# Kernel tuning notes

Measured on AMD Instinct MI355X. Metric: run time of the kernel, lower is better.

The kernel has to match this reference:

```python
import jax, jax.numpy as jnp
import numpy as np

B, D, NT, NZ = 16384, 64, 128, 2048


def setup_inputs() -> dict:
    key = jax.random.key(0)
    ks = jax.random.split(key, 5)
    return {
        "t": jax.random.uniform(ks[0], (1,), dtype=jnp.float32),
        "z": jax.random.normal(ks[1], (B, D), dtype=jnp.float32),
        "logp_z": jnp.zeros((B, 1), jnp.float32),
        "centres_z": jax.random.normal(ks[2], (NZ, D), dtype=jnp.float32),
        "log_sigmas_z": jnp.zeros((NZ,), jnp.float32),
        "centres_t": jax.random.normal(ks[3], (NT, 1), dtype=jnp.float32),
        "log_sigmas_t": jnp.zeros((NT,), jnp.float32),
        "W": 0.01 * jax.random.normal(ks[4], (D, NT, NZ + 1), dtype=jnp.float32),
    }


def _gauss(r):
    return jnp.exp(-r * r)


def _forward(t, z, centres_z, log_sigmas_z, centres_t, log_sigmas_t, W):
    # time RBF features Phi_t: (NT,)
    r_t = jnp.abs(t.reshape(1, 1) - centres_t.reshape(1, -1)) / jnp.exp(log_sigmas_t)
    phi_t = _gauss(r_t).reshape(-1)
    W_t = jnp.einsum('dij,i->dj', W, phi_t)  # (D, NZ+1)
    Wz, bias = W_t[:, :-1], W_t[:, -1]       # bias comes from the appended ones column
    # z RBF features via squared-distance identity (avoids [B,NZ,D] blowup)
    sq = (jnp.sum(z * z, axis=1, keepdims=True)
          + jnp.sum(centres_z * centres_z, axis=1)[None, :]
          - 2.0 * z @ centres_z.T)
    sq = jnp.maximum(sq, 0.0)                 # (B, NZ) squared distances
    inv_s2 = jnp.exp(-2.0 * log_sigmas_z)     # 1/sigma_j^2, (NZ,)
    phi_z = jnp.exp(-sq * inv_s2)             # gaussian(||z-c_j||/s_j), (B, NZ)
    dz_dt = phi_z @ Wz.T + bias               # (B, D)
    # exact Jacobian trace for gaussian basis:
    #   d phi_j / d z_i = -2 * phi_j * (z_i - c_{j,i}) / s_j^2
    #   tr(J)_b = sum_j phi_{b,j} * inv_s2_j * (-2) * (sum_i Wz[i,j] z_{b,i} - sum_i Wz[i,j] c_{j,i})
    q = jnp.einsum('dj,jd->j', Wz, centres_z)  # (NZ,)
    trace = -2.0 * jnp.sum(phi_z * inv_s2 * (z @ Wz - q), axis=1)  # (B,)
    dlogp_z_dt = -trace[:, None]               # (B, 1)
    return dz_dt, dlogp_z_dt


def reference(t, z, logp_z, centres_z, log_sigmas_z, centres_t, log_sigmas_t, W):
    return _forward(t, z, centres_z, log_sigmas_z, centres_t, log_sigmas_t, W)
```

## Files before the change

kernel.cpp:

```cpp
#include <hip/hip_runtime.h>
#include <math.h>

typedef unsigned int uint;
typedef unsigned short ushort;
typedef unsigned char uchar;
typedef __attribute__((ext_vector_type(4))) float f32x4;

#define BB  16384
#define DD  64
#define NT_ 128
#define NZ_ 2048
#define NJ_ 2049

#define BIAS_OFF 0
#define SCS_OFF  64
#define ZF8A_OFF 8256
#define ZF8B_OFF 139328
#define ZZG_OFF  270400
#define CZ8A_OFF 286784
#define CZ8B_OFF 303168
#define WZ8A_OFF 319552
#define WZ8B_OFF 335936
#define WZBP_OFF 352320
#define PART_OFF 417856

#if __has_builtin(__builtin_amdgcn_cvt_pk_fp8_f32)
__device__ __forceinline__ uint pk4_fp8(float a, float b, float c, float d) {
  int v = __builtin_amdgcn_cvt_pk_fp8_f32(a, b, 0, false);
  v = __builtin_amdgcn_cvt_pk_fp8_f32(c, d, v, true);
  return (uint)v;
}
__device__ __forceinline__ uchar f8_1(float x) {
  return (uchar)(__builtin_amdgcn_cvt_pk_fp8_f32(x, x, 0, false) & 0xFF);
}
#else
__device__ __forceinline__ uint sw_f8(float x) {
  uint u = __float_as_uint(x);
  uint s = (u >> 24) & 0x80u;
  float ax = __uint_as_float(u & 0x7FFFFFFFu);
  if (!(ax >= 0.015625f)) return s;
  if (ax >= 448.f) return s | 0x7Eu;
  uint q = __float_as_uint(ax);
  q += 0x7FFFFu + ((q >> 20) & 1u);
  uint e = (q >> 23) - 120u;
  return s | ((e & 0xFu) << 3) | ((q >> 20) & 7u);
}
__device__ __forceinline__ uchar f8_1(float x) { return (uchar)sw_f8(x); }
__device__ __forceinline__ uint pk4_fp8(float a, float b, float c, float d) {
  return sw_f8(a) | (sw_f8(b) << 8) | (sw_f8(c) << 16) | (sw_f8(d) << 24);
}
#endif

__global__ __launch_bounds__(256) void k_wt1(
    const float* __restrict__ t, const float* __restrict__ ct,
    const float* __restrict__ lst, const float* __restrict__ W,
    float* __restrict__ part)
{
  __shared__ float ph[32];
  int tx = threadIdx.x;
  int d  = blockIdx.y;
  int ic = blockIdx.z;
  if (tx < 32) {
    int i = ic * 32 + tx;
    float r = fabsf(t[0] - ct[i]) * __expf(-lst[i]);
    ph[tx] = __expf(-r * r);
  }
  __syncthreads();
  int j = blockIdx.x * 256 + tx;
  if (j >= NJ_) return;
  const float* Wp = W + (size_t)d * NT_ * NJ_ + (size_t)(ic * 32) * NJ_ + j;
  float acc = 0.f;
#pragma unroll
  for (int k = 0; k < 32; ++k) acc += Wp[(size_t)k * NJ_] * ph[k];
  part[((size_t)ic * 64 + d) * NJ_ + j] = acc;
}

__global__ __launch_bounds__(256) void k_prep2(
    const float* __restrict__ part, const float* __restrict__ cz,
    const float* __restrict__ lsz,
    float* __restrict__ bias, float4* __restrict__ scs,
    uchar* __restrict__ cz8a, uchar* __restrict__ cz8b,
    uchar* __restrict__ wz8a, uchar* __restrict__ wz8b,
    uchar* __restrict__ wzbp8)
{
  __shared__ float wt[64][9];
  int tid = threadIdx.x;
  int cb0 = blockIdx.x * 8;
#pragma unroll
  for (int h = 0; h < 2; ++h) {
    int f = h * 256 + tid;
    int d = f >> 3, c = f & 7;
    size_t idx = (size_t)d * NJ_ + cb0 + c;
    float s = part[idx] + part[(size_t)64 * NJ_ + idx]
            + part[(size_t)128 * NJ_ + idx] + part[(size_t)192 * NJ_ + idx];
    wt[d][c] = s;
    int cg = cb0 + c;
    wzbp8[((size_t)(cg >> 5) * 64 + d) * 32 + (cg & 31)] = f8_1(s);
  }
  if (blockIdx.x == 0 && tid < 64) {
    size_t idx = (size_t)tid * NJ_ + 2048;
    bias[tid] = part[idx] + part[(size_t)64 * NJ_ + idx]
              + part[(size_t)128 * NJ_ + idx] + part[(size_t)192 * NJ_ + idx];
  }
  __syncthreads();
  int cl = tid >> 5;
  int k  = tid & 31;
  int c  = cb0 + cl;
  float cv0 = cz[(size_t)c * DD + k];
  float cv1 = cz[(size_t)c * DD + 32 + k];
  cz8a[(size_t)c * 32 + k] = f8_1(cv0);
  cz8b[(size_t)c * 32 + k] = f8_1(cv1);
  float w0 = wt[k][cl], w1 = wt[32 + k][cl];
  wz8a[(size_t)c * 32 + k] = f8_1(w0);
  wz8b[(size_t)c * 32 + k] = f8_1(w1);
  float ca = cv0 * cv0 + cv1 * cv1;
  float qa = w0 * cv0 + w1 * cv1;
  qa += __shfl_xor(qa, 1);  ca += __shfl_xor(ca, 1);
  qa += __shfl_xor(qa, 2);  ca += __shfl_xor(ca, 2);
  qa += __shfl_xor(qa, 4);  ca += __shfl_xor(ca, 4);
  qa += __shfl_xor(qa, 8);  ca += __shfl_xor(ca, 8);
  qa += __shfl_xor(qa, 16); ca += __shfl_xor(ca, 16);
  if (k == 0) scs[c] = make_float4(ca, __expf(-2.f * lsz[c]), qa, 0.f);
}

__global__ __launch_bounds__(256) void k_zbp(
    const float* __restrict__ z, uchar* __restrict__ zf8a,
    uchar* __restrict__ zf8b, float* __restrict__ zzg)
{
  int g = blockIdx.x * 256 + threadIdx.x;
  int r = g >> 3, s8 = g & 7;
  const float4* zp = (const float4*)(z + (size_t)r * DD + s8 * 8);
  float4 v0 = zp[0], v1 = zp[1];
  uint lo = pk4_fp8(v0.x, v0.y, v0.z, v0.w);
  uint hi = pk4_fp8(v1.x, v1.y, v1.z, v1.w);
  uchar* dst = (s8 < 4 ? zf8a : zf8b) + (size_t)r * 32 + (s8 & 3) * 8;
  *(uint2*)dst = make_uint2(lo, hi);
  float ss = v0.x * v0.x + v0.y * v0.y + v0.z * v0.z + v0.w * v0.w
           + v1.x * v1.x + v1.y * v1.y + v1.z * v1.z + v1.w * v1.w;
  ss += __shfl_xor(ss, 1);
  ss += __shfl_xor(ss, 2);
  ss += __shfl_xor(ss, 4);
  if (s8 == 0) zzg[r] = ss;
}

#define PH_LD 40

__global__ __launch_bounds__(256) void k_fused(
    const uchar* __restrict__ zf8a, const uchar* __restrict__ zf8b,
    const float* __restrict__ zzg,
    const uchar* __restrict__ cz8a, const uchar* __restrict__ cz8b,
    const uchar* __restrict__ wz8a, const uchar* __restrict__ wz8b,
    const uchar* __restrict__ wzbp8,
    const float4* __restrict__ scs, const float* __restrict__ bias,
    float* __restrict__ out)
{
  __shared__ char smem[10240];
  __shared__ float dlr[4][32];
  uchar* phs = (uchar*)smem;
  float* eps = (float*)smem;

  int tid  = threadIdx.x;
  int ws   = tid >> 6;
  int lane = tid & 63;
  int lrow = lane & 15, quad = lane >> 4;
  int b0 = blockIdx.x * 32;

  long az[2][2];
#pragma unroll
  for (int mt = 0; mt < 2; ++mt) {
    size_t ro = (size_t)(b0 + mt * 16 + lrow) * 32 + quad * 8;
    az[mt][0] = *(const long*)(zf8a + ro);
    az[mt][1] = *(const long*)(zf8b + ro);
  }
  float zzr[2][4];
#pragma unroll
  for (int mt = 0; mt < 2; ++mt) {
    float v = zzg[b0 + mt * 16 + lrow];
#pragma unroll
    for (int i = 0; i < 4; ++i) zzr[mt][i] = __shfl(v, quad * 4 + i);
  }

  f32x4 acc[2][4];
#pragma unroll
  for (int mt = 0; mt < 2; ++mt)
#pragma unroll
    for (int nt = 0; nt < 4; ++nt) acc[mt][nt] = (f32x4){0.f, 0.f, 0.f, 0.f};
  float dl[2][4] = {{0.f}};

  const f32x4 zero = (f32x4){0.f, 0.f, 0.f, 0.f};
  int cbase = ws * 512;
  int pbase = ws * 32 * PH_LD;

  long Abc0[2][2], Abc1[2][2], Abw0[2][2], Abw1[2][2], Abb[2][4];
  float4 Asc[2][2];
#define LOADB(PAR, C0)                                                         \
  do {                                                                         \
    int c0_ = (C0);                                                            \
    _Pragma("unroll")                                                          \
    for (int nt = 0; nt < 2; ++nt) {                                           \
      int cg_ = c0_ + nt * 16 + lrow;                                          \
      size_t ro_ = (size_t)cg_ * 32 + quad * 8;                                \
      Abc0[PAR][nt] = *(const long*)(cz8a + ro_);                              \
      Abc1[PAR][nt] = *(const long*)(cz8b + ro_);                              \
      Abw0[PAR][nt] = *(const long*)(wz8a + ro_);                              \
      Abw1[PAR][nt] = *(const long*)(wz8b + ro_);                              \
      Asc[PAR][nt]  = scs[cg_];                                                \
    }                                                                          \
    size_t cb_ = (size_t)(c0_ >> 5) * 64 * 32;                                 \
    _Pragma("unroll")                                                          \
    for (int nt = 0; nt < 4; ++nt)                                             \
      Abb[PAR][nt] =                                                           \
          *(const long*)(wzbp8 + cb_ + (size_t)(nt * 16 + lrow) * 32 + quad * 8); \
  } while (0)

  LOADB(0, cbase);
#pragma unroll 2
  for (int it = 0; it < 16; ++it) {
    int par = it & 1;
    LOADB(par ^ 1, cbase + ((it + 1) & 15) * 32);

    int pb = par * (4 * 32 * PH_LD) + pbase;
#pragma unroll
    for (int nt = 0; nt < 2; ++nt) {
      float4 sc = Asc[par][nt];
#pragma unroll
      for (int mt = 0; mt < 2; ++mt) {
        f32x4 d1 = __builtin_amdgcn_mfma_f32_16x16x32_fp8_fp8(az[mt][0], Abc0[par][nt], zero, 0, 0, 0);
        d1       = __builtin_amdgcn_mfma_f32_16x16x32_fp8_fp8(az[mt][1], Abc1[par][nt], d1,   0, 0, 0);
        f32x4 d2 = __builtin_amdgcn_mfma_f32_16x16x32_fp8_fp8(az[mt][0], Abw0[par][nt], zero, 0, 0, 0);
        d2       = __builtin_amdgcn_mfma_f32_16x16x32_fp8_fp8(az[mt][1], Abw1[par][nt], d2,   0, 0, 0);
#pragma unroll
        for (int i = 0; i < 4; ++i) {
          float s = zzr[mt][i] + sc.x - 2.f * d1[i];
          s = fmaxf(s, 0.f);
          float p = __expf(-s * sc.y);
          dl[mt][i] += p * sc.y * (d2[i] - sc.z);
          phs[pb + (mt * 16 + quad * 4 + i) * PH_LD + nt * 16 + lrow] = f8_1(p);
        }
      }
    }
    long ap0 = *(const long*)&phs[pb + lrow * PH_LD + quad * 8];
    long ap1 = *(const long*)&phs[pb + (16 + lrow) * PH_LD + quad * 8];
#pragma unroll
    for (int nt = 0; nt < 4; ++nt) {
      acc[0][nt] = __builtin_amdgcn_mfma_f32_16x16x32_fp8_fp8(ap0, Abb[par][nt], acc[0][nt], 0, 0, 0);
      acc[1][nt] = __builtin_amdgcn_mfma_f32_16x16x32_fp8_fp8(ap1, Abb[par][nt], acc[1][nt], 0, 0, 0);
    }
  }
#undef LOADB

#pragma unroll
  for (int mt = 0; mt < 2; ++mt)
#pragma unroll
    for (int i = 0; i < 4; ++i) {
      float v = dl[mt][i];
      v += __shfl_xor(v, 1);
      v += __shfl_xor(v, 2);
      v += __shfl_xor(v, 4);
      v += __shfl_xor(v, 8);
      if (lrow == 0) dlr[ws][mt * 16 + quad * 4 + i] = v;
    }

  for (int s = 0; s < 4; ++s) {
    __syncthreads();
    if (ws == s) {
#pragma unroll
      for (int mt = 0; mt < 2; ++mt)
#pragma unroll
        for (int nt = 0; nt < 4; ++nt)
#pragma unroll
          for (int i = 0; i < 4; ++i) {
            int r = mt * 16 + quad * 4 + i;
            int d = nt * 16 + lrow;
            if (s == 0) eps[r * 68 + d] = acc[mt][nt][i];
            else        eps[r * 68 + d] += acc[mt][nt][i];
          }
    }
  }
  __syncthreads();

  {
    int r = tid >> 3, d0 = (tid & 7) * 8;
    float4 e0 = *(const float4*)&eps[r * 68 + d0];
    float4 e1 = *(const float4*)&eps[r * 68 + d0 + 4];
    float4 bv0 = *(const float4*)&bias[d0];
    float4 bv1 = *(const float4*)&bias[d0 + 4];
    float4 o0, o1;
    o0.x = e0.x + bv0.x; o0.y = e0.y + bv0.y; o0.z = e0.z + bv0.z; o0.w = e0.w + bv0.w;
    o1.x = e1.x + bv1.x; o1.y = e1.y + bv1.y; o1.z = e1.z + bv1.z; o1.w = e1.w + bv1.w;
    *(float4*)&out[(size_t)(b0 + r) * DD + d0]     = o0;
    *(float4*)&out[(size_t)(b0 + r) * DD + d0 + 4] = o1;
  }
  if (tid < 32) {
    float s = dlr[0][tid] + dlr[1][tid] + dlr[2][tid] + dlr[3][tid];
    out[(size_t)BB * DD + b0 + tid] = 2.f * s;
  }
}

extern "C" void kernel_launch(void* const* d_in, const int* in_sizes, int n_in,
                              void* d_out, int out_size, void* d_ws, size_t ws_size,
                              hipStream_t stream)
{
  const float* t   = (const float*)d_in[0];
  const float* z   = (const float*)d_in[1];
  const float* cz  = (const float*)d_in[3];
  const float* lsz = (const float*)d_in[4];
  const float* ct  = (const float*)d_in[5];
  const float* lst = (const float*)d_in[6];
  const float* W   = (const float*)d_in[7];
  float* out = (float*)d_out;
  float* ws  = (float*)d_ws;

  float*  bias = ws + BIAS_OFF;
  float4* scs  = (float4*)(ws + SCS_OFF);
  uchar*  zf8a = (uchar*)(ws + ZF8A_OFF);
  uchar*  zf8b = (uchar*)(ws + ZF8B_OFF);
  float*  zzg  = ws + ZZG_OFF;
  uchar*  cz8a = (uchar*)(ws + CZ8A_OFF);
  uchar*  cz8b = (uchar*)(ws + CZ8B_OFF);
  uchar*  wz8a = (uchar*)(ws + WZ8A_OFF);
  uchar*  wz8b = (uchar*)(ws + WZ8B_OFF);
  uchar*  wzbp8 = (uchar*)(ws + WZBP_OFF);
  float*  part = ws + PART_OFF;

  k_wt1<<<dim3(9, 64, 4), 256, 0, stream>>>(t, ct, lst, W, part);
  k_prep2<<<dim3(256), 256, 0, stream>>>(part, cz, lsz, bias, scs,
                                         cz8a, cz8b, wz8a, wz8b, wzbp8);
  k_zbp<<<dim3(512), 256, 0, stream>>>(z, zf8a, zf8b, zzg);
  k_fused<<<dim3(BB / 32), 256, 0, stream>>>(zf8a, zf8b, zzg, cz8a, cz8b,
                                             wz8a, wz8b, wzbp8, scs, bias, out);
}
```

Baseline: 141.2 us.

## Fuse z fp8 packing into main kernel and halve rows per block

Removes the separate k_zbp pass. The main kernel now loads fp32 z directly, converts it to fp8 in registers and computes row norms with cross-quad shuffles, which drops a launch and a workspace round-trip. It also halves the batch tile from 32 to 16 rows per block, doubling the grid and shrinking shared memory and register state. The trade-off is that each centre and weight fragment is reused across only 16 rows, so L2 and global traffic for the fp8 centre and weight data roughly doubles.

After: 151.3 us. 1.07x slower.

```diff
diff --git a/kernel.cpp b/kernel.cpp
--- a/kernel.cpp
+++ b/kernel.cpp
@@ -2,7 +2,7 @@
 #include <math.h>
 
 typedef unsigned int uint;
-typedef unsigned short ushort;
+typedef unsigned long ulong;
 typedef unsigned char uchar;
 typedef __attribute__((ext_vector_type(4))) float f32x4;
 
@@ -14,15 +14,12 @@
 
 #define BIAS_OFF 0
 #define SCS_OFF  64
-#define ZF8A_OFF 8256
-#define ZF8B_OFF 139328
-#define ZZG_OFF  270400
-#define CZ8A_OFF 286784
-#define CZ8B_OFF 303168
-#define WZ8A_OFF 319552
-#define WZ8B_OFF 335936
-#define WZBP_OFF 352320
-#define PART_OFF 417856
+#define CZ8A_OFF 8256
+#define CZ8B_OFF 24640
+#define WZ8A_OFF 41024
+#define WZ8B_OFF 57408
+#define WZBP_OFF 73792
+#define PART_OFF 106560
 
 #if __has_builtin(__builtin_amdgcn_cvt_pk_fp8_f32)
 __device__ __forceinline__ uint pk4_fp8(float a, float b, float c, float d) {
@@ -123,39 +120,18 @@
   if (k == 0) scs[c] = make_float4(ca, __expf(-2.f * lsz[c]), qa, 0.f);
 }
 
-__global__ __launch_bounds__(256) void k_zbp(
-    const float* __restrict__ z, uchar* __restrict__ zf8a,
-    uchar* __restrict__ zf8b, float* __restrict__ zzg)
-{
-  int g = blockIdx.x * 256 + threadIdx.x;
-  int r = g >> 3, s8 = g & 7;
-  const float4* zp = (const float4*)(z + (size_t)r * DD + s8 * 8);
-  float4 v0 = zp[0], v1 = zp[1];
-  uint lo = pk4_fp8(v0.x, v0.y, v0.z, v0.w);
-  uint hi = pk4_fp8(v1.x, v1.y, v1.z, v1.w);
-  uchar* dst = (s8 < 4 ? zf8a : zf8b) + (size_t)r * 32 + (s8 & 3) * 8;
-  *(uint2*)dst = make_uint2(lo, hi);
-  float ss = v0.x * v0.x + v0.y * v0.y + v0.z * v0.z + v0.w * v0.w
-           + v1.x * v1.x + v1.y * v1.y + v1.z * v1.z + v1.w * v1.w;
-  ss += __shfl_xor(ss, 1);
-  ss += __shfl_xor(ss, 2);
-  ss += __shfl_xor(ss, 4);
-  if (s8 == 0) zzg[r] = ss;
-}
-
 #define PH_LD 40
 
 __global__ __launch_bounds__(256) void k_fused(
-    const uchar* __restrict__ zf8a, const uchar* __restrict__ zf8b,
-    const float* __restrict__ zzg,
+    const float* __restrict__ z,
     const uchar* __restrict__ cz8a, const uchar* __restrict__ cz8b,
     const uchar* __restrict__ wz8a, const uchar* __restrict__ wz8b,
     const uchar* __restrict__ wzbp8,
     const float4* __restrict__ scs, const float* __restrict__ bias,
     float* __restrict__ out)
 {
-  __shared__ char smem[10240];
-  __shared__ float dlr[4][32];
+  __shared__ char smem[5376];
+  __shared__ float dlr[4][16];
   uchar* phs = (uchar*)smem;
   float* eps = (float*)smem;
 
@@ -163,33 +139,40 @@
   int ws   = tid >> 6;
   int lane = tid & 63;
   int lrow = lane & 15, quad = lane >> 4;
-  int b0 = blockIdx.x * 32;
-
-  long az[2][2];
-#pragma unroll
-  for (int mt = 0; mt < 2; ++mt) {
-    size_t ro = (size_t)(b0 + mt * 16 + lrow) * 32 + quad * 8;
-    az[mt][0] = *(const long*)(zf8a + ro);
-    az[mt][1] = *(const long*)(zf8b + ro);
-  }
-  float zzr[2][4];
-#pragma unroll
-  for (int mt = 0; mt < 2; ++mt) {
-    float v = zzg[b0 + mt * 16 + lrow];
-#pragma unroll
-    for (int i = 0; i < 4; ++i) zzr[mt][i] = __shfl(v, quad * 4 + i);
-  }
-
-  f32x4 acc[2][4];
-#pragma unroll
-  for (int mt = 0; mt < 2; ++mt)
-#pragma unroll
-    for (int nt = 0; nt < 4; ++nt) acc[mt][nt] = (f32x4){0.f, 0.f, 0.f, 0.f};
-  float dl[2][4] = {{0.f}};
+  int b0 = blockIdx.x * 16;
+
+  long az[2];
+  float zzr[4];
+  {
+    const float* zr = z + (size_t)(b0 + lrow) * DD + quad * 8;
+    float4 u0 = *(const float4*)(zr);
+    float4 u1 = *(const float4*)(zr + 4);
+    float4 u2 = *(const float4*)(zr + 32);
+    float4 u3 = *(const float4*)(zr + 36);
+    uint l0 = pk4_fp8(u0.x, u0.y, u0.z, u0.w);
+    uint h0 = pk4_fp8(u1.x, u1.y, u1.z, u1.w);
+    uint l1 = pk4_fp8(u2.x, u2.y, u2.z, u2.w);
+    uint h1 = pk4_fp8(u3.x, u3.y, u3.z, u3.w);
+    az[0] = (long)((ulong)l0 | ((ulong)h0 << 32));
+    az[1] = (long)((ulong)l1 | ((ulong)h1 << 32));
+    float p = u0.x*u0.x + u0.y*u0.y + u0.z*u0.z + u0.w*u0.w
+            + u1.x*u1.x + u1.y*u1.y + u1.z*u1.z + u1.w*u1.w
+            + u2.x*u2.x + u2.y*u2.y + u2.z*u2.z + u2.w*u2.w
+            + u3.x*u3.x + u3.y*u3.y + u3.z*u3.z + u3.w*u3.w;
+    p += __shfl_xor(p, 16);
+    p += __shfl_xor(p, 32);
+#pragma unroll
+    for (int i = 0; i < 4; ++i) zzr[i] = __shfl(p, quad * 4 + i);
+  }
+
+  f32x4 acc[4];
+#pragma unroll
+  for (int nt = 0; nt < 4; ++nt) acc[nt] = (f32x4){0.f, 0.f, 0.f, 0.f};
+  float dl[4] = {0.f, 0.f, 0.f, 0.f};
 
   const f32x4 zero = (f32x4){0.f, 0.f, 0.f, 0.f};
   int cbase = ws * 512;
-  int pbase = ws * 32 * PH_LD;
+  int pbase = ws * 16 * PH_LD;
 
   long Abc0[2][2], Abc1[2][2], Abw0[2][2], Abw1[2][2], Abb[2][4];
   float4 Asc[2][2];
@@ -219,79 +202,65 @@
     int par = it & 1;
     LOADB(par ^ 1, cbase + ((it + 1) & 15) * 32);
 
-    int pb = par * (4 * 32 * PH_LD) + pbase;
+    int pb = par * (4 * 16 * PH_LD) + pbase;
 #pragma unroll
     for (int nt = 0; nt < 2; ++nt) {
       float4 sc = Asc[par][nt];
-#pragma unroll
-      for (int mt = 0; mt < 2; ++mt) {
-        f32x4 d1 = __builtin_amdgcn_mfma_f32_16x16x32_fp8_fp8(az[mt][0], Abc0[par][nt], zero, 0, 0, 0);
-        d1       = __builtin_amdgcn_mfma_f32_16x16x32_fp8_fp8(az[mt][1], Abc1[par][nt], d1,   0, 0, 0);
-        f32x4 d2 = __builtin_amdgcn_mfma_f32_16x16x32_fp8_fp8(az[mt][0], Abw0[par][nt], zero, 0, 0, 0);
-        d2       = __builtin_amdgcn_mfma_f32_16x16x32_fp8_fp8(az[mt][1], Abw1[par][nt], d2,   0, 0, 0);
-#pragma unroll
-        for (int i = 0; i < 4; ++i) {
-          float s = zzr[mt][i] + sc.x - 2.f * d1[i];
-          s = fmaxf(s, 0.f);
-          float p = __expf(-s * sc.y);
-          dl[mt][i] += p * sc.y * (d2[i] - sc.z);
-          phs[pb + (mt * 16 + quad * 4 + i) * PH_LD + nt * 16 + lrow] = f8_1(p);
-        }
+      f32x4 d1 = __builtin_amdgcn_mfma_f32_16x16x32_fp8_fp8(az[0], Abc0[par][nt], zero, 0, 0, 0);
+      d1       = __builtin_amdgcn_mfma_f32_16x16x32_fp8_fp8(az[1], Abc1[par][nt], d1,   0, 0, 0);
+      f32x4 d2 = __builtin_amdgcn_mfma_f32_16x16x32_fp8_fp8(az[0], Abw0[par][nt], zero, 0, 0, 0);
+      d2       = __builtin_amdgcn_mfma_f32_16x16x32_fp8_fp8(az[1], Abw1[par][nt], d2,   0, 0, 0);
+#pragma unroll
+      for (int i = 0; i < 4; ++i) {
+        float s = zzr[i] + sc.x - 2.f * d1[i];
+        s = fmaxf(s, 0.f);
+        float p = __expf(-s * sc.y);
+        dl[i] += p * sc.y * (d2[i] - sc.z);
+        phs[pb + (quad * 4 + i) * PH_LD + nt * 16 + lrow] = f8_1(p);
       }
     }
-    long ap0 = *(const long*)&phs[pb + lrow * PH_LD + quad * 8];
-    long ap1 = *(const long*)&phs[pb + (16 + lrow) * PH_LD + quad * 8];
-#pragma unroll
-    for (int nt = 0; nt < 4; ++nt) {
-      acc[0][nt] = __builtin_amdgcn_mfma_f32_16x16x32_fp8_fp8(ap0, Abb[par][nt], acc[0][nt], 0, 0, 0);
-      acc[1][nt] = __builtin_amdgcn_mfma_f32_16x16x32_fp8_fp8(ap1, Abb[par][nt], acc[1][nt], 0, 0, 0);
-    }
+    long ap = *(const long*)&phs[pb + lrow * PH_LD + quad * 8];
+#pragma unroll
+    for (int nt = 0; nt < 4; ++nt)
+      acc[nt] = __builtin_amdgcn_mfma_f32_16x16x32_fp8_fp8(ap, Abb[par][nt], acc[nt], 0, 0, 0);
   }
 #undef LOADB
 
 #pragma unroll
-  for (int mt = 0; mt < 2; ++mt)
-#pragma unroll
-    for (int i = 0; i < 4; ++i) {
-      float v = dl[mt][i];
-      v += __shfl_xor(v, 1);
-      v += __shfl_xor(v, 2);
-      v += __shfl_xor(v, 4);
-      v += __shfl_xor(v, 8);
-      if (lrow == 0) dlr[ws][mt * 16 + quad * 4 + i] = v;
-    }
+  for (int i = 0; i < 4; ++i) {
+    float v = dl[i];
+    v += __shfl_xor(v, 1);
+    v += __shfl_xor(v, 2);
+    v += __shfl_xor(v, 4);
+    v += __shfl_xor(v, 8);
+    if (lrow == 0) dlr[ws][quad * 4 + i] = v;
+  }
 
   for (int s = 0; s < 4; ++s) {
     __syncthreads();
     if (ws == s) {
 #pragma unroll
-      for (int mt = 0; mt < 2; ++mt)
-#pragma unroll
-        for (int nt = 0; nt < 4; ++nt)
-#pragma unroll
-          for (int i = 0; i < 4; ++i) {
-            int r = mt * 16 + quad * 4 + i;
-            int d = nt * 16 + lrow;
-            if (s == 0) eps[r * 68 + d] = acc[mt][nt][i];
-            else        eps[r * 68 + d] += acc[mt][nt][i];
-          }
+      for (int nt = 0; nt < 4; ++nt)
+#pragma unroll
+        for (int i = 0; i < 4; ++i) {
+          int r = quad * 4 + i;
+          int d = nt * 16 + lrow;
+          if (s == 0) eps[r * 68 + d] = acc[nt][i];
+          else        eps[r * 68 + d] += acc[nt][i];
+        }
     }
   }
   __syncthreads();
 
   {
-    int r = tid >> 3, d0 = (tid & 7) * 8;
-    float4 e0 = *(const float4*)&eps[r * 68 + d0];
-    float4 e1 = *(const float4*)&eps[r * 68 + d0 + 4];
-    float4 bv0 = *(const float4*)&bias[d0];
-    float4 bv1 = *(const float4*)&bias[d0 + 4];
-    float4 o0, o1;
-    o0.x = e0.x + bv0.x; o0.y = e0.y + bv0.y; o0.z = e0.z + bv0.z; o0.w = e0.w + bv0.w;
-    o1.x = e1.x + bv1.x; o1.y = e1.y + bv1.y; o1.z = e1.z + bv1.z; o1.w = e1.w + bv1.w;
-    *(float4*)&out[(size_t)(b0 + r) * DD + d0]     = o0;
-    *(float4*)&out[(size_t)(b0 + r) * DD + d0 + 4] = o1;
-  }
-  if (tid < 32) {
+    int r = tid >> 4, d0 = (tid & 15) * 4;
+    float4 e  = *(const float4*)&eps[r * 68 + d0];
+    float4 bv = *(const float4*)&bias[d0];
+    float4 o;
+    o.x = e.x + bv.x; o.y = e.y + bv.y; o.z = e.z + bv.z; o.w = e.w + bv.w;
+    *(float4*)&out[(size_t)(b0 + r) * DD + d0] = o;
+  }
+  if (tid < 16) {
     float s = dlr[0][tid] + dlr[1][tid] + dlr[2][tid] + dlr[3][tid];
     out[(size_t)BB * DD + b0 + tid] = 2.f * s;
   }
@@ -313,9 +282,6 @@
 
   float*  bias = ws + BIAS_OFF;
   float4* scs  = (float4*)(ws + SCS_OFF);
-  uchar*  zf8a = (uchar*)(ws + ZF8A_OFF);
-  uchar*  zf8b = (uchar*)(ws + ZF8B_OFF);
-  float*  zzg  = ws + ZZG_OFF;
   uchar*  cz8a = (uchar*)(ws + CZ8A_OFF);
   uchar*  cz8b = (uchar*)(ws + CZ8B_OFF);
   uchar*  wz8a = (uchar*)(ws + WZ8A_OFF);
@@ -326,7 +292,6 @@
   k_wt1<<<dim3(9, 64, 4), 256, 0, stream>>>(t, ct, lst, W, part);
   k_prep2<<<dim3(256), 256, 0, stream>>>(part, cz, lsz, bias, scs,
                                          cz8a, cz8b, wz8a, wz8b, wzbp8);
-  k_zbp<<<dim3(512), 256, 0, stream>>>(z, zf8a, zf8b, zzg);
-  k_fused<<<dim3(BB / 32), 256, 0, stream>>>(zf8a, zf8b, zzg, cz8a, cz8b,
-                                             wz8a, wz8b, wzbp8, scs, bias, out);
-}
+  k_fused<<<dim3(BB / 16), 256, 0, stream>>>(z, cz8a, cz8b, wz8a, wz8b,
+                                             wzbp8, scs, bias, out);
+}
```

## Fuse z fp8 packing into main kernel and transpose MFMA operands for packed stores

Applied to the files above, without the earlier changes.

Removes the separate z-conversion kernel: the fused kernel now reads fp32 z directly, packs it to fp8 and computes row norms in registers. It swaps the MFMA A/B operands so each lane holds four consecutive centres for one row, which allows per-centre constants to be loaded as float4 vectors and the phi values to be stored to LDS as packed 32-bit words instead of single bytes. The float4 struct-of-params layout is split into separate arrays, and the main loop is fully unrolled. This saves one launch and a workspace round-trip at the cost of more redundant z loads per block and higher register pressure.

Measured after the change: 176.1 us. 1.25x slower.

```diff
diff --git a/kernel.cpp b/kernel.cpp
--- a/kernel.cpp
+++ b/kernel.cpp
@@ -2,9 +2,10 @@
 #include <math.h>
 
 typedef unsigned int uint;
-typedef unsigned short ushort;
+typedef unsigned long ulong;
 typedef unsigned char uchar;
 typedef __attribute__((ext_vector_type(4))) float f32x4;
+typedef uint __attribute__((may_alias)) uint_a;
 
 #define BB  16384
 #define DD  64
@@ -13,16 +14,15 @@
 #define NJ_ 2049
 
 #define BIAS_OFF 0
-#define SCS_OFF  64
-#define ZF8A_OFF 8256
-#define ZF8B_OFF 139328
-#define ZZG_OFF  270400
-#define CZ8A_OFF 286784
-#define CZ8B_OFF 303168
-#define WZ8A_OFF 319552
-#define WZ8B_OFF 335936
-#define WZBP_OFF 352320
-#define PART_OFF 417856
+#define CCS_OFF  64
+#define INVS_OFF 2112
+#define QS_OFF   4160
+#define CZ8A_OFF 6208
+#define CZ8B_OFF 22592
+#define WZ8A_OFF 38976
+#define WZ8B_OFF 55360
+#define WZBP_OFF 71744
+#define PART_OFF 104512
 
 #if __has_builtin(__builtin_amdgcn_cvt_pk_fp8_f32)
 __device__ __forceinline__ uint pk4_fp8(float a, float b, float c, float d) {
@@ -78,7 +78,8 @@
 __global__ __launch_bounds__(256) void k_prep2(
     const float* __restrict__ part, const float* __restrict__ cz,
     const float* __restrict__ lsz,
-    float* __restrict__ bias, float4* __restrict__ scs,
+    float* __restrict__ bias, float* __restrict__ ccs,
+    float* __restrict__ invs, float* __restrict__ qs,
     uchar* __restrict__ cz8a, uchar* __restrict__ cz8b,
     uchar* __restrict__ wz8a, uchar* __restrict__ wz8b,
     uchar* __restrict__ wzbp8)
@@ -120,38 +121,22 @@
   qa += __shfl_xor(qa, 4);  ca += __shfl_xor(ca, 4);
   qa += __shfl_xor(qa, 8);  ca += __shfl_xor(ca, 8);
   qa += __shfl_xor(qa, 16); ca += __shfl_xor(ca, 16);
-  if (k == 0) scs[c] = make_float4(ca, __expf(-2.f * lsz[c]), qa, 0.f);
-}
-
-__global__ __launch_bounds__(256) void k_zbp(
-    const float* __restrict__ z, uchar* __restrict__ zf8a,
-    uchar* __restrict__ zf8b, float* __restrict__ zzg)
-{
-  int g = blockIdx.x * 256 + threadIdx.x;
-  int r = g >> 3, s8 = g & 7;
-  const float4* zp = (const float4*)(z + (size_t)r * DD + s8 * 8);
-  float4 v0 = zp[0], v1 = zp[1];
-  uint lo = pk4_fp8(v0.x, v0.y, v0.z, v0.w);
-  uint hi = pk4_fp8(v1.x, v1.y, v1.z, v1.w);
-  uchar* dst = (s8 < 4 ? zf8a : zf8b) + (size_t)r * 32 + (s8 & 3) * 8;
-  *(uint2*)dst = make_uint2(lo, hi);
-  float ss = v0.x * v0.x + v0.y * v0.y + v0.z * v0.z + v0.w * v0.w
-           + v1.x * v1.x + v1.y * v1.y + v1.z * v1.z + v1.w * v1.w;
-  ss += __shfl_xor(ss, 1);
-  ss += __shfl_xor(ss, 2);
-  ss += __shfl_xor(ss, 4);
-  if (s8 == 0) zzg[r] = ss;
+  if (k == 0) {
+    ccs[c]  = ca;
+    invs[c] = __expf(-2.f * lsz[c]);
+    qs[c]   = qa;
+  }
 }
 
 #define PH_LD 40
 
 __global__ __launch_bounds__(256) void k_fused(
-    const uchar* __restrict__ zf8a, const uchar* __restrict__ zf8b,
-    const float* __restrict__ zzg,
+    const float* __restrict__ z,
     const uchar* __restrict__ cz8a, const uchar* __restrict__ cz8b,
     const uchar* __restrict__ wz8a, const uchar* __restrict__ wz8b,
     const uchar* __restrict__ wzbp8,
-    const float4* __restrict__ scs, const float* __restrict__ bias,
+    const float* __restrict__ ccs, const float* __restrict__ invs,
+    const float* __restrict__ qs, const float* __restrict__ bias,
     float* __restrict__ out)
 {
   __shared__ char smem[10240];
@@ -166,18 +151,27 @@
   int b0 = blockIdx.x * 32;
 
   long az[2][2];
+  float zzs[2];
 #pragma unroll
   for (int mt = 0; mt < 2; ++mt) {
-    size_t ro = (size_t)(b0 + mt * 16 + lrow) * 32 + quad * 8;
-    az[mt][0] = *(const long*)(zf8a + ro);
-    az[mt][1] = *(const long*)(zf8b + ro);
-  }
-  float zzr[2][4];
-#pragma unroll
-  for (int mt = 0; mt < 2; ++mt) {
-    float v = zzg[b0 + mt * 16 + lrow];
-#pragma unroll
-    for (int i = 0; i < 4; ++i) zzr[mt][i] = __shfl(v, quad * 4 + i);
+    const float* zr = z + (size_t)(b0 + mt * 16 + lrow) * DD;
+    float4 u0 = *(const float4*)(zr + quad * 8);
+    float4 u1 = *(const float4*)(zr + quad * 8 + 4);
+    float4 u2 = *(const float4*)(zr + 32 + quad * 8);
+    float4 u3 = *(const float4*)(zr + 32 + quad * 8 + 4);
+    uint l0 = pk4_fp8(u0.x, u0.y, u0.z, u0.w);
+    uint h0 = pk4_fp8(u1.x, u1.y, u1.z, u1.w);
+    uint l1 = pk4_fp8(u2.x, u2.y, u2.z, u2.w);
+    uint h1 = pk4_fp8(u3.x, u3.y, u3.z, u3.w);
+    az[mt][0] = (long)((ulong)l0 | ((ulong)h0 << 32));
+    az[mt][1] = (long)((ulong)l1 | ((ulong)h1 << 32));
+    float p = u0.x*u0.x + u0.y*u0.y + u0.z*u0.z + u0.w*u0.w
+            + u1.x*u1.x + u1.y*u1.y + u1.z*u1.z + u1.w*u1.w
+            + u2.x*u2.x + u2.y*u2.y + u2.z*u2.z + u2.w*u2.w
+            + u3.x*u3.x + u3.y*u3.y + u3.z*u3.z + u3.w*u3.w;
+    p += __shfl_xor(p, 16);
+    p += __shfl_xor(p, 32);
+    zzs[mt] = p;
   }
 
   f32x4 acc[2][4];
@@ -185,14 +179,13 @@
   for (int mt = 0; mt < 2; ++mt)
 #pragma unroll
     for (int nt = 0; nt < 4; ++nt) acc[mt][nt] = (f32x4){0.f, 0.f, 0.f, 0.f};
-  float dl[2][4] = {{0.f}};
+  float dl[2] = {0.f, 0.f};
 
   const f32x4 zero = (f32x4){0.f, 0.f, 0.f, 0.f};
   int cbase = ws * 512;
-  int pbase = ws * 32 * PH_LD;
+  int pwave = ws * 2 * 16 * PH_LD;
 
   long Abc0[2][2], Abc1[2][2], Abw0[2][2], Abw1[2][2], Abb[2][4];
-  float4 Asc[2][2];
 #define LOADB(PAR, C0)                                                         \
   do {                                                                         \
     int c0_ = (C0);                                                            \
@@ -204,7 +197,6 @@
       Abc1[PAR][nt] = *(const long*)(cz8b + ro_);                              \
       Abw0[PAR][nt] = *(const long*)(wz8a + ro_);                              \
       Abw1[PAR][nt] = *(const long*)(wz8b + ro_);                              \
-      Asc[PAR][nt]  = scs[cg_];                                                \
     }                                                                          \
     size_t cb_ = (size_t)(c0_ >> 5) * 64 * 32;                                 \
     _Pragma("unroll")                                                          \
@@ -214,52 +206,62 @@
   } while (0)
 
   LOADB(0, cbase);
-#pragma unroll 2
+#pragma unroll
   for (int it = 0; it < 16; ++it) {
-    int par = it & 1;
-    LOADB(par ^ 1, cbase + ((it + 1) & 15) * 32);
-
-    int pb = par * (4 * 32 * PH_LD) + pbase;
+    const int par = it & 1;
+    const int c0 = cbase + it * 32;
+    LOADB(par ^ 1, (it == 15) ? cbase : (c0 + 32));
+
+    const int pb = par * 5120 + pwave;
 #pragma unroll
     for (int nt = 0; nt < 2; ++nt) {
-      float4 sc = Asc[par][nt];
+      int cs = c0 + nt * 16 + quad * 4;
+      f32x4 cc4 = *(const f32x4*)(ccs + cs);
+      f32x4 iv4 = *(const f32x4*)(invs + cs);
+      f32x4 q4  = *(const f32x4*)(qs + cs);
 #pragma unroll
       for (int mt = 0; mt < 2; ++mt) {
-        f32x4 d1 = __builtin_amdgcn_mfma_f32_16x16x32_fp8_fp8(az[mt][0], Abc0[par][nt], zero, 0, 0, 0);
-        d1       = __builtin_amdgcn_mfma_f32_16x16x32_fp8_fp8(az[mt][1], Abc1[par][nt], d1,   0, 0, 0);
-        f32x4 d2 = __builtin_amdgcn_mfma_f32_16x16x32_fp8_fp8(az[mt][0], Abw0[par][nt], zero, 0, 0, 0);
-        d2       = __builtin_amdgcn_mfma_f32_16x16x32_fp8_fp8(az[mt][1], Abw1[par][nt], d2,   0, 0, 0);
-#pragma unroll
-        for (int i = 0; i < 4; ++i) {
-          float s = zzr[mt][i] + sc.x - 2.f * d1[i];
-          s = fmaxf(s, 0.f);
-          float p = __expf(-s * sc.y);
-          dl[mt][i] += p * sc.y * (d2[i] - sc.z);
-          phs[pb + (mt * 16 + quad * 4 + i) * PH_LD + nt * 16 + lrow] = f8_1(p);
-        }
+        f32x4 d1 = __builtin_amdgcn_mfma_f32_16x16x32_fp8_fp8(Abc0[par][nt], az[mt][0], zero, 0, 0, 0);
+        d1       = __builtin_amdgcn_mfma_f32_16x16x32_fp8_fp8(Abc1[par][nt], az[mt][1], d1,   0, 0, 0);
+        f32x4 d2 = __builtin_amdgcn_mfma_f32_16x16x32_fp8_fp8(Abw0[par][nt], az[mt][0], zero, 0, 0, 0);
+        d2       = __builtin_amdgcn_mfma_f32_16x16x32_fp8_fp8(Abw1[par][nt], az[mt][1], d2,   0, 0, 0);
+        float zz = zzs[mt];
+        float s0 = fmaxf(fmaf(-2.f, d1[0], zz + cc4[0]), 0.f);
+        float s1 = fmaxf(fmaf(-2.f, d1[1], zz + cc4[1]), 0.f);
+        float s2 = fmaxf(fmaf(-2.f, d1[2], zz + cc4[2]), 0.f);
+        float s3 = fmaxf(fmaf(-2.f, d1[3], zz + cc4[3]), 0.f);
+        float p0 = __expf(-s0 * iv4[0]);
+        float p1 = __expf(-s1 * iv4[1]);
+        float p2 = __expf(-s2 * iv4[2]);
+        float p3 = __expf(-s3 * iv4[3]);
+        dl[mt] += p0 * iv4[0] * (d2[0] - q4[0])
+                + p1 * iv4[1] * (d2[1] - q4[1])
+                + p2 * iv4[2] * (d2[2] - q4[2])
+                + p3 * iv4[3] * (d2[3] - q4[3]);
+        uint_a* pw = (uint_a*)(phs + pb + (mt * 16 + lrow) * PH_LD);
+        pw[nt * 4 + quad] = pk4_fp8(p0, p1, p2, p3);
       }
     }
-    long ap0 = *(const long*)&phs[pb + lrow * PH_LD + quad * 8];
-    long ap1 = *(const long*)&phs[pb + (16 + lrow) * PH_LD + quad * 8];
-#pragma unroll
-    for (int nt = 0; nt < 4; ++nt) {
-      acc[0][nt] = __builtin_amdgcn_mfma_f32_16x16x32_fp8_fp8(ap0, Abb[par][nt], acc[0][nt], 0, 0, 0);
-      acc[1][nt] = __builtin_amdgcn_mfma_f32_16x16x32_fp8_fp8(ap1, Abb[par][nt], acc[1][nt], 0, 0, 0);
+#pragma unroll
+    for (int mt = 0; mt < 2; ++mt) {
+      const uint_a* pr = (const uint_a*)(phs + pb + (mt * 16 + lrow) * PH_LD);
+      uint plo = pr[quad * 2];
+      uint phi_ = pr[quad * 2 + 1];
+      long ap = (long)((ulong)plo | ((ulong)phi_ << 32));
+#pragma unroll
+      for (int nt = 0; nt < 4; ++nt)
+        acc[mt][nt] = __builtin_amdgcn_mfma_f32_16x16x32_fp8_fp8(ap, Abb[par][nt], acc[mt][nt], 0, 0, 0);
     }
   }
 #undef LOADB
 
 #pragma unroll
-  for (int mt = 0; mt < 2; ++mt)
-#pragma unroll
-    for (int i = 0; i < 4; ++i) {
-      float v = dl[mt][i];
-      v += __shfl_xor(v, 1);
-      v += __shfl_xor(v, 2);
-      v += __shfl_xor(v, 4);
-      v += __shfl_xor(v, 8);
-      if (lrow == 0) dlr[ws][mt * 16 + quad * 4 + i] = v;
-    }
+  for (int mt = 0; mt < 2; ++mt) {
+    float v = dl[mt];
+    v += __shfl_xor(v, 16);
+    v += __shfl_xor(v, 32);
+    if (quad == 0) dlr[ws][mt * 16 + lrow] = v;
+  }
 
   for (int s = 0; s < 4; ++s) {
     __syncthreads();
@@ -312,10 +314,9 @@
   float* ws  = (float*)d_ws;
 
   float*  bias = ws + BIAS_OFF;
-  float4* scs  = (float4*)(ws + SCS_OFF);
-  uchar*  zf8a = (uchar*)(ws + ZF8A_OFF);
-  uchar*  zf8b = (uchar*)(ws + ZF8B_OFF);
-  float*  zzg  = ws + ZZG_OFF;
+  float*  ccs  = ws + CCS_OFF;
+  float*  invs = ws + INVS_OFF;
+  float*  qs   = ws + QS_OFF;
   uchar*  cz8a = (uchar*)(ws + CZ8A_OFF);
   uchar*  cz8b = (uchar*)(ws + CZ8B_OFF);
   uchar*  wz8a = (uchar*)(ws + WZ8A_OFF);
@@ -324,9 +325,8 @@
   float*  part = ws + PART_OFF;
 
   k_wt1<<<dim3(9, 64, 4), 256, 0, stream>>>(t, ct, lst, W, part);
-  k_prep2<<<dim3(256), 256, 0, stream>>>(part, cz, lsz, bias, scs,
+  k_prep2<<<dim3(256), 256, 0, stream>>>(part, cz, lsz, bias, ccs, invs, qs,
                                          cz8a, cz8b, wz8a, wz8b, wzbp8);
-  k_zbp<<<dim3(512), 256, 0, stream>>>(z, zf8a, zf8b, zzg);
-  k_fused<<<dim3(BB / 32), 256, 0, stream>>>(zf8a, zf8b, zzg, cz8a, cz8b,
-                                             wz8a, wz8b, wzbp8, scs, bias, out);
-}
+  k_fused<<<dim3(BB / 32), 256, 0, stream>>>(z, cz8a, cz8b, wz8a, wz8b,
+                                             wzbp8, ccs, invs, qs, bias, out);
+}
```
